# Kernel tuning notes

Measured on AMD Instinct MI355X. Metric: run time of the kernel, lower is better.

## Reference

```python
import jax, jax.numpy as jnp
import numpy as np

EPS = 1e-12  # matches F.normalize default eps

def _angle(e):
    # e: [N, D] embeddings
    d = e[:, None, :] - e[None, :, :]                      # [N, N, D] pairwise differences
    n = jnp.linalg.norm(d, axis=-1, keepdims=True)         # [N, N, 1]
    d = d / jnp.maximum(n, EPS)                            # normalized diffs; diagonal stays 0
    # all-triplet cosines: for each anchor i, Gram matrix of its normalized diffs
    return jnp.einsum('ijd,ikd->ijk', d, d)                # [N, N, N]

def _smooth_l1_mean(a, b):
    # torch F.smooth_l1_loss with beta=1.0, reduction='mean'
    x = jnp.abs(a - b)
    return jnp.mean(jnp.where(x < 1.0, 0.5 * x * x, x - 0.5))

def setup_inputs() -> dict:
    key = jax.random.key(0)
    k1, k2 = jax.random.split(key)
    student = jax.random.normal(k1, (384, 256), dtype=jnp.float32)
    teacher = jax.random.normal(k2, (384, 256), dtype=jnp.float32)
    return {"student": student, "teacher": teacher}

def reference(student, teacher):
    s_angle = _angle(student)
    t_angle = _angle(teacher)
    return _smooth_l1_mean(s_angle, t_angle)
```

## Files before the change

### kernel.cpp

```cpp
#include <hip/hip_runtime.h>

#define NPTS 384
#define DIMS 256
#define TI 6
#define JC 24

__global__ __launch_bounds__(64) void gram_pack_kernel(
        const float* __restrict__ Es, const float* __restrict__ Et,
        float2* __restrict__ Ps, float2* __restrict__ Pt,
        float* __restrict__ Ws, float* __restrict__ Wt,
        float* __restrict__ out) {
    const float* __restrict__ E = (blockIdx.z == 0) ? Es : Et;
    float2* __restrict__ P      = (blockIdx.z == 0) ? Ps : Pt;
    float* __restrict__ W       = (blockIdx.z == 0) ? Ws : Wt;

    if (blockIdx.x == 0 && blockIdx.y == 0 && blockIdx.z == 0 && threadIdx.x == 0)
        out[0] = 0.0f;

    __shared__ float AsT[32][36];
    __shared__ float BsT[32][36];
    __shared__ float dA[32];
    __shared__ float dB[32];

    const int t  = threadIdx.x;
    const int tx = t & 7;
    const int ty = t >> 3;
    const int i0 = blockIdx.x * 32;
    const int j0 = blockIdx.y * 32;

    const int e = t & 31;
    const float* dsrc = (t < 32) ? &AsT[0][e] : &BsT[0][e];
    float dsum = 0.0f;

    float acc[4][4] = {};

    for (int k0 = 0; k0 < DIMS; k0 += 32) {
#pragma unroll
        for (int m = 0; m < 4; m++) {
            const int row = ty + 8 * m;
            float va[4], vb[4];
            *(float4*)va = *(const float4*)&E[(i0 + row) * DIMS + k0 + 4 * tx];
            *(float4*)vb = *(const float4*)&E[(j0 + row) * DIMS + k0 + 4 * tx];
#pragma unroll
            for (int q = 0; q < 4; q++) {
                AsT[4 * tx + q][row] = va[q];
                BsT[4 * tx + q][row] = vb[q];
            }
        }
        __syncthreads();
#pragma unroll
        for (int k = 0; k < 32; k++) {
            float a[4], b[4];
            *(float4*)a = *(const float4*)&AsT[k][4 * ty];
            *(float4*)b = *(const float4*)&BsT[k][4 * tx];
#pragma unroll
            for (int p = 0; p < 4; p++)
#pragma unroll
                for (int q = 0; q < 4; q++)
                    acc[p][q] = fmaf(a[p], b[q], acc[p][q]);
        }
#pragma unroll
        for (int k = 0; k < 32; k++) {
            float v = dsrc[k * 36];
            dsum = fmaf(v, v, dsum);
        }
        __syncthreads();
    }

    if (t < 32) dA[e] = dsum; else dB[e] = dsum;
    __syncthreads();

#pragma unroll
    for (int p = 0; p < 4; p++) {
        const int i   = i0 + 4 * ty + p;
        const float dAv = dA[4 * ty + p];
        float2 prow[4];
        float  wrow[4];
#pragma unroll
        for (int q = 0; q < 4; q++) {
            const int j   = j0 + 4 * tx + q;
            const float g   = acc[p][q];
            const float dBv = dB[4 * tx + q];
            float v = fmaxf(dAv - 2.0f * g + dBv, 0.0f);
            float r = (i == j) ? 0.0f : 1.0f / fmaxf(sqrtf(v), 1e-12f);
            prow[q] = make_float2(dAv - g, r);
            wrow[q] = g;
        }
        *(float4*)&P[i * NPTS + j0 + 4 * tx]     = make_float4(prow[0].x, prow[0].y, prow[1].x, prow[1].y);
        *(float4*)&P[i * NPTS + j0 + 4 * tx + 2] = make_float4(prow[2].x, prow[2].y, prow[3].x, prow[3].y);
        *(float4*)&W[i * NPTS + j0 + 4 * tx]     = make_float4(wrow[0], wrow[1], wrow[2], wrow[3]);
    }
}

__global__ __launch_bounds__(NPTS) void rkd_angle_kernel(
        const float2* __restrict__ Ps, const float2* __restrict__ Pt,
        const float* __restrict__ Ws, const float* __restrict__ Wt,
        float* __restrict__ out) {
    const int k  = threadIdx.x;
    const int i0 = blockIdx.x * TI;
    const int j0 = blockIdx.y * JC;

    float rsk[TI], rtk[TI], nqs[TI], nqt[TI];
#pragma unroll
    for (int r = 0; r < TI; r++) {
        float2 ps = Ps[(i0 + r) * NPTS + k];
        float2 pt = Pt[(i0 + r) * NPTS + k];
        float  ws = Ws[(i0 + r) * NPTS + k];
        float  wt = Wt[(i0 + r) * NPTS + k];
        rsk[r] = ps.y;
        rtk[r] = pt.y;
        nqs[r] = -(ps.y * ws);
        nqt[r] = -(pt.y * wt);
    }

    float acc = 0.0f;
#pragma unroll 2
    for (int j = j0; j < j0 + JC; j++) {
        float ws = Ws[j * NPTS + k];
        float wt = Wt[j * NPTS + k];
#pragma unroll
        for (int r = 0; r < TI; r++) {
            float2 pjs = Ps[(i0 + r) * NPTS + j];
            float2 pjt = Pt[(i0 + r) * NPTS + j];
            float as = pjs.y * fmaf(rsk[r], ws + pjs.x, nqs[r]);
            float at = pjt.y * fmaf(rtk[r], wt + pjt.x, nqt[r]);
            float d  = as - at;
            float ad = fabsf(d);
            float m  = fminf(ad, 1.0f);
            acc = fmaf(m, fmaf(-0.5f, m, ad), acc);
        }
    }

#pragma unroll
    for (int off = 32; off > 0; off >>= 1)
        acc += __shfl_down(acc, off, 64);

    __shared__ float wsum[NPTS / 64];
    const int wid  = k >> 6;
    const int lane = k & 63;
    if (lane == 0) wsum[wid] = acc;
    __syncthreads();
    if (k == 0) {
        float s = 0.0f;
#pragma unroll
        for (int w = 0; w < NPTS / 64; w++) s += wsum[w];
        atomicAdd(out, s * (1.0f / (384.0f * 384.0f * 384.0f)));
    }
}

extern "C" void kernel_launch(void* const* d_in, const int* in_sizes, int n_in,
                              void* d_out, int out_size, void* d_ws, size_t ws_size,
                              hipStream_t stream) {
    const float* student = (const float*)d_in[0];
    const float* teacher = (const float*)d_in[1];
    float* out = (float*)d_out;

    float2* Ps = (float2*)d_ws;
    float2* Pt = Ps + NPTS * NPTS;
    float*  Ws = (float*)(Pt + NPTS * NPTS);
    float*  Wt = Ws + NPTS * NPTS;

    dim3 ggrid(NPTS / 32, NPTS / 32, 2);
    gram_pack_kernel<<<ggrid, 64, 0, stream>>>(student, teacher, Ps, Pt, Ws, Wt, out);

    dim3 mgrid(NPTS / TI, NPTS / JC, 1);
    rkd_angle_kernel<<<mgrid, NPTS, 0, stream>>>(Ps, Pt, Ws, Wt, out);
}
```

Before: 93.17 us.

## Interleave student/teacher packed buffers and split Gram K-loop across six waves

The Gram kernel now runs 384-thread blocks in which six waves each take a slice of the K dimension into private LDS tiles. The partial results are reduced in shared memory, and wave 0 writes the outputs. Student and teacher results are interleaved into float4/float2 buffers, so the triplet kernel needs one wide load instead of two or four scalar loads per element. The triplet grid is flattened with JC doubled to 48, giving fewer blocks and fewer atomics. The trade-offs are uneven K work (8 chunks over 6 waves), a serial reduction and epilogue on one wave, and strided scalar stores into the interleaved layout.

```diff
diff --git a/kernel.cpp b/kernel.cpp
--- a/kernel.cpp
+++ b/kernel.cpp
@@ -3,38 +3,45 @@
 #define NPTS 384
 #define DIMS 256
 #define TI 6
-#define JC 24
+#define JC 48
+#define NW 6
+#define NBLK 512
+#define NTILES 288
 
-__global__ __launch_bounds__(64) void gram_pack_kernel(
+__global__ __launch_bounds__(NPTS) void gram_pack_kernel(
         const float* __restrict__ Es, const float* __restrict__ Et,
-        float2* __restrict__ Ps, float2* __restrict__ Pt,
-        float* __restrict__ Ws, float* __restrict__ Wt,
+        float4* __restrict__ P4, float2* __restrict__ W2,
         float* __restrict__ out) {
-    const float* __restrict__ E = (blockIdx.z == 0) ? Es : Et;
-    float2* __restrict__ P      = (blockIdx.z == 0) ? Ps : Pt;
-    float* __restrict__ W       = (blockIdx.z == 0) ? Ws : Wt;
+    __shared__ float SA[NW][32][36];
+    __shared__ float SB[NW][32][36];
+    __shared__ float dpart[NW][64];
+    __shared__ float dAB[64];
 
-    if (blockIdx.x == 0 && blockIdx.y == 0 && blockIdx.z == 0 && threadIdx.x == 0)
-        out[0] = 0.0f;
+    const int tid  = threadIdx.x;
+    const int w    = tid >> 6;
+    const int lane = tid & 63;
 
-    __shared__ float AsT[32][36];
-    __shared__ float BsT[32][36];
-    __shared__ float dA[32];
-    __shared__ float dB[32];
+    if (blockIdx.x == 0 && tid == 0) out[0] = 0.0f;
 
-    const int t  = threadIdx.x;
-    const int tx = t & 7;
-    const int ty = t >> 3;
-    const int i0 = blockIdx.x * 32;
-    const int j0 = blockIdx.y * 32;
+    const int tb  = blockIdx.x;
+    const int z   = tb / 144;
+    const int rem = tb - z * 144;
+    const int ti  = rem / 12;
+    const int tj  = rem - ti * 12;
+    const int i0  = ti * 32;
+    const int j0  = tj * 32;
+    const float* __restrict__ E = z ? Et : Es;
 
-    const int e = t & 31;
-    const float* dsrc = (t < 32) ? &AsT[0][e] : &BsT[0][e];
+    const int tx = lane & 7;
+    const int ty = lane >> 3;
+    const int e  = lane & 31;
+    const float* dsrc = (lane < 32) ? &SA[w][0][e] : &SB[w][0][e];
+
+    float acc[4][4] = {};
     float dsum = 0.0f;
 
-    float acc[4][4] = {};
-
-    for (int k0 = 0; k0 < DIMS; k0 += 32) {
+    for (int c = w; c < 8; c += NW) {
+        const int k0 = c * 32;
 #pragma unroll
         for (int m = 0; m < 4; m++) {
             const int row = ty + 8 * m;
@@ -43,16 +50,17 @@
             *(float4*)vb = *(const float4*)&E[(j0 + row) * DIMS + k0 + 4 * tx];
 #pragma unroll
             for (int q = 0; q < 4; q++) {
-                AsT[4 * tx + q][row] = va[q];
-                BsT[4 * tx + q][row] = vb[q];
+                SA[w][4 * tx + q][row] = va[q];
+                SB[w][4 * tx + q][row] = vb[q];
             }
         }
-        __syncthreads();
+        asm volatile("s_waitcnt lgkmcnt(0)" ::: "memory");
+
 #pragma unroll
-        for (int k = 0; k < 32; k++) {
+        for (int kk = 0; kk < 32; kk++) {
             float a[4], b[4];
-            *(float4*)a = *(const float4*)&AsT[k][4 * ty];
-            *(float4*)b = *(const float4*)&BsT[k][4 * tx];
+            *(float4*)a = *(const float4*)&SA[w][kk][4 * ty];
+            *(float4*)b = *(const float4*)&SB[w][kk][4 * tx];
 #pragma unroll
             for (int p = 0; p < 4; p++)
 #pragma unroll
@@ -60,70 +68,87 @@
                     acc[p][q] = fmaf(a[p], b[q], acc[p][q]);
         }
 #pragma unroll
-        for (int k = 0; k < 32; k++) {
-            float v = dsrc[k * 36];
+        for (int kk = 0; kk < 32; kk++) {
+            float v = dsrc[kk * 36];
             dsum = fmaf(v, v, dsum);
         }
-        __syncthreads();
+        asm volatile("s_waitcnt lgkmcnt(0)" ::: "memory");
     }
 
-    if (t < 32) dA[e] = dsum; else dB[e] = dsum;
+    {
+        float* pb = &SA[w][0][0];
+#pragma unroll
+        for (int p = 0; p < 4; p++)
+            *(float4*)&pb[lane * 16 + 4 * p] =
+                make_float4(acc[p][0], acc[p][1], acc[p][2], acc[p][3]);
+        dpart[w][lane] = dsum;
+    }
     __syncthreads();
 
+    if (w == 0) {
 #pragma unroll
-    for (int p = 0; p < 4; p++) {
-        const int i   = i0 + 4 * ty + p;
-        const float dAv = dA[4 * ty + p];
-        float2 prow[4];
-        float  wrow[4];
+        for (int ww = 1; ww < NW; ww++) {
+            const float* qb = &SA[ww][0][0];
 #pragma unroll
-        for (int q = 0; q < 4; q++) {
-            const int j   = j0 + 4 * tx + q;
-            const float g   = acc[p][q];
-            const float dBv = dB[4 * tx + q];
-            float v = fmaxf(dAv - 2.0f * g + dBv, 0.0f);
-            float r = (i == j) ? 0.0f : 1.0f / fmaxf(sqrtf(v), 1e-12f);
-            prow[q] = make_float2(dAv - g, r);
-            wrow[q] = g;
+            for (int p = 0; p < 4; p++) {
+                float4 v = *(const float4*)&qb[lane * 16 + 4 * p];
+                acc[p][0] += v.x; acc[p][1] += v.y;
+                acc[p][2] += v.z; acc[p][3] += v.w;
+            }
         }
-        *(float4*)&P[i * NPTS + j0 + 4 * tx]     = make_float4(prow[0].x, prow[0].y, prow[1].x, prow[1].y);
-        *(float4*)&P[i * NPTS + j0 + 4 * tx + 2] = make_float4(prow[2].x, prow[2].y, prow[3].x, prow[3].y);
-        *(float4*)&W[i * NPTS + j0 + 4 * tx]     = make_float4(wrow[0], wrow[1], wrow[2], wrow[3]);
+        float dtot = 0.0f;
+#pragma unroll
+        for (int ww = 0; ww < NW; ww++) dtot += dpart[ww][lane];
+        dAB[lane] = dtot;
+        asm volatile("s_waitcnt lgkmcnt(0)" ::: "memory");
+
+#pragma unroll
+        for (int p = 0; p < 4; p++) {
+            const int i     = i0 + 4 * ty + p;
+            const float dAv = dAB[4 * ty + p];
+#pragma unroll
+            for (int q = 0; q < 4; q++) {
+                const int j     = j0 + 4 * tx + q;
+                const float g   = acc[p][q];
+                const float dBv = dAB[32 + 4 * tx + q];
+                float v = fmaxf(dAv - 2.0f * g + dBv, 0.0f);
+                float r = (i == j) ? 0.0f : 1.0f / fmaxf(sqrtf(v), 1e-12f);
+                float* dstP = (float*)&P4[i * NPTS + j];
+                float* dstW = (float*)&W2[i * NPTS + j];
+                *(float2*)(dstP + 2 * z) = make_float2(dAv - g, r);
+                dstW[z] = g;
+            }
+        }
     }
 }
 
 __global__ __launch_bounds__(NPTS) void rkd_angle_kernel(
-        const float2* __restrict__ Ps, const float2* __restrict__ Pt,
-        const float* __restrict__ Ws, const float* __restrict__ Wt,
+        const float4* __restrict__ P4, const float2* __restrict__ W2,
         float* __restrict__ out) {
     const int k  = threadIdx.x;
-    const int i0 = blockIdx.x * TI;
-    const int j0 = blockIdx.y * JC;
+    const int i0 = (blockIdx.x >> 3) * TI;
+    const int j0 = (blockIdx.x & 7) * JC;
 
     float rsk[TI], rtk[TI], nqs[TI], nqt[TI];
 #pragma unroll
     for (int r = 0; r < TI; r++) {
-        float2 ps = Ps[(i0 + r) * NPTS + k];
-        float2 pt = Pt[(i0 + r) * NPTS + k];
-        float  ws = Ws[(i0 + r) * NPTS + k];
-        float  wt = Wt[(i0 + r) * NPTS + k];
-        rsk[r] = ps.y;
-        rtk[r] = pt.y;
-        nqs[r] = -(ps.y * ws);
-        nqt[r] = -(pt.y * wt);
+        float4 pk = P4[(i0 + r) * NPTS + k];
+        float2 wk = W2[(i0 + r) * NPTS + k];
+        rsk[r] = pk.y;
+        rtk[r] = pk.w;
+        nqs[r] = -(pk.y * wk.x);
+        nqt[r] = -(pk.w * wk.y);
     }
 
     float acc = 0.0f;
 #pragma unroll 2
     for (int j = j0; j < j0 + JC; j++) {
-        float ws = Ws[j * NPTS + k];
-        float wt = Wt[j * NPTS + k];
+        float2 wv = W2[j * NPTS + k];
 #pragma unroll
         for (int r = 0; r < TI; r++) {
-            float2 pjs = Ps[(i0 + r) * NPTS + j];
-            float2 pjt = Pt[(i0 + r) * NPTS + j];
-            float as = pjs.y * fmaf(rsk[r], ws + pjs.x, nqs[r]);
-            float at = pjt.y * fmaf(rtk[r], wt + pjt.x, nqt[r]);
+            float4 pj = P4[(i0 + r) * NPTS + j];
+            float as = pj.y * fmaf(rsk[r], wv.x + pj.x, nqs[r]);
+            float at = pj.w * fmaf(rtk[r], wv.y + pj.z, nqt[r]);
             float d  = as - at;
             float ad = fabsf(d);
             float m  = fminf(ad, 1.0f);
@@ -135,15 +160,14 @@
     for (int off = 32; off > 0; off >>= 1)
         acc += __shfl_down(acc, off, 64);
 
-    __shared__ float wsum[NPTS / 64];
-    const int wid  = k >> 6;
-    const int lane = k & 63;
-    if (lane == 0) wsum[wid] = acc;
+    __shared__ float wsum[NW];
+    const int w = k >> 6, lane = k & 63;
+    if (lane == 0) wsum[w] = acc;
     __syncthreads();
     if (k == 0) {
         float s = 0.0f;
 #pragma unroll
-        for (int w = 0; w < NPTS / 64; w++) s += wsum[w];
+        for (int ww = 0; ww < NW; ww++) s += wsum[ww];
         atomicAdd(out, s * (1.0f / (384.0f * 384.0f * 384.0f)));
     }
 }
@@ -155,14 +179,9 @@
     const float* teacher = (const float*)d_in[1];
     float* out = (float*)d_out;
 
-    float2* Ps = (float2*)d_ws;
-    float2* Pt = Ps + NPTS * NPTS;
-    float*  Ws = (float*)(Pt + NPTS * NPTS);
-    float*  Wt = Ws + NPTS * NPTS;
+    float4* P4 = (float4*)d_ws;
+    float2* W2 = (float2*)(P4 + NPTS * NPTS);
 
-    dim3 ggrid(NPTS / 32, NPTS / 32, 2);
-    gram_pack_kernel<<<ggrid, 64, 0, stream>>>(student, teacher, Ps, Pt, Ws, Wt, out);
-
-    dim3 mgrid(NPTS / TI, NPTS / JC, 1);
-    rkd_angle_kernel<<<mgrid, NPTS, 0, stream>>>(Ps, Pt, Ws, Wt, out);
+    gram_pack_kernel<<<dim3(NTILES), NPTS, 0, stream>>>(student, teacher, P4, W2, out);
+    rkd_angle_kernel<<<dim3(NBLK), NPTS, 0, stream>>>(P4, W2, out);
 }
```

After: 100.5 us. 7.9% more time.
